# Optimization experiments

Hardware: AMD Instinct MI355X
Metric: run time of the kernel (lower is better)

## Reference

```python
import jax, jax.numpy as jnp
import numpy as np

EPS = 1e-5

def layer_norm(x, g, b):
    mu = jnp.mean(x, axis=-1, keepdims=True)
    var = jnp.var(x, axis=-1, keepdims=True)
    return (x - mu) * jax.lax.rsqrt(var + EPS) * g + b

def setup_inputs() -> dict:
    key = jax.random.key(0)
    ks = jax.random.split(key, 9)
    B, S, E = 16, 2048, 512
    H = 2 * E
    q = jax.random.normal(ks[0], (B, S, E), dtype=jnp.float32)
    k = jax.random.normal(ks[1], (B, S, E), dtype=jnp.float32)
    v = jax.random.normal(ks[2], (B, S, E), dtype=jnp.float32)
    # LayerNorm params (norm1 and norm3; norm2 is dead code in the original)
    ln1_g = jnp.ones((E,), jnp.float32); ln1_b = jnp.zeros((E,), jnp.float32)
    ln3_g = jnp.ones((E,), jnp.float32); ln3_b = jnp.zeros((E,), jnp.float32)
    # FFN params, torch Linear default init (uniform +- 1/sqrt(fan_in))
    lim1 = 1.0 / np.sqrt(E)
    w1 = jax.random.uniform(ks[3], (E, H), jnp.float32, -lim1, lim1)
    b1 = jax.random.uniform(ks[4], (H,), jnp.float32, -lim1, lim1)
    lim2 = 1.0 / np.sqrt(H)
    w2 = jax.random.uniform(ks[5], (H, E), jnp.float32, -lim2, lim2)
    b2 = jax.random.uniform(ks[6], (E,), jnp.float32, -lim2, lim2)
    return {"q": q, "k": k, "v": v, "ln1_g": ln1_g, "ln1_b": ln1_b,
            "w1": w1, "b1": b1, "w2": w2, "b2": b2,
            "ln3_g": ln3_g, "ln3_b": ln3_b}

def reference(q, k, v, ln1_g, ln1_b, w1, b1, w2, b2, ln3_g, ln3_b):
    # single-head full attention: scores [B,S,S]
    scale = 1.0 / jnp.sqrt(jnp.asarray(q.shape[-1], q.dtype))
    scores = jnp.einsum('bse,bte->bst', q, k) * scale
    attn = jax.nn.softmax(scores, axis=-1)
    attn_out = jnp.einsum('bst,bte->bse', attn, v)
    # residual + LayerNorm (dropout is identity at p=0 / eval)
    x = layer_norm(q + attn_out, ln1_g, ln1_b)
    # FFN: Linear -> exact GELU -> Linear
    h = jax.nn.gelu(jnp.einsum('bse,eh->bsh', x, w1) + b1, approximate=False)
    ff = jnp.einsum('bsh,he->bse', h, w2) + b2
    return layer_norm(x + ff, ln3_g, ln3_b)
```

## Files before the change

kernel.cpp:

```cpp
#include <hip/hip_runtime.h>
#include <cstdint>

#define B_ 16
#define S_ 2048
#define E_ 512
#define H_ 1024
#define SCALE 0.044194173824159216f
#define KVB 32
#define NTILES 64

typedef __attribute__((ext_vector_type(8))) short short8;
typedef __attribute__((ext_vector_type(4))) float floatx4;

static __device__ __forceinline__ unsigned short f2bf(float f) {
    unsigned u = __float_as_uint(f);
    u = u + 0x7FFFu + ((u >> 16) & 1u);
    return (unsigned short)(u >> 16);
}
static __device__ __forceinline__ float bf2f(unsigned short h) {
    return __uint_as_float(((unsigned)h) << 16);
}

__global__ void cvt_f32_bf16(const float* __restrict__ in, unsigned short* __restrict__ out, int n8) {
    int i = blockIdx.x * blockDim.x + threadIdx.x;
    if (i >= n8) return;
    const float4* p = (const float4*)in + (long)i * 2;
    float4 a = p[0], b = p[1];
    union { unsigned short u[8]; uint4 v; } r;
    r.u[0] = f2bf(a.x); r.u[1] = f2bf(a.y); r.u[2] = f2bf(a.z); r.u[3] = f2bf(a.w);
    r.u[4] = f2bf(b.x); r.u[5] = f2bf(b.y); r.u[6] = f2bf(b.z); r.u[7] = f2bf(b.w);
    ((uint4*)out)[i] = r.v;
}

__global__ void transpose_cvt(const float* __restrict__ in, unsigned short* __restrict__ out,
                              int R, int C, long inBS, long outBS) {
    __shared__ float t[64 * 68];
    const int z = blockIdx.z;
    in += (long)z * inBS; out += (long)z * outBS;
    const int c0 = blockIdx.x * 64, r0 = blockIdx.y * 64;
    const int tid = threadIdx.x;
    {
        int col4 = (tid & 15) * 4;
        #pragma unroll
        for (int i = 0; i < 4; i++) {
            int row = (tid >> 4) + i * 16;
            float4 v = *(const float4*)(in + (long)(r0 + row) * C + c0 + col4);
            *(float4*)(&t[row * 68 + col4]) = v;
        }
    }
    __syncthreads();
    {
        int oc = tid >> 2;
        int ob = (tid & 3) * 16;
        union { unsigned short u[16]; uint4 v[2]; } r;
        #pragma unroll
        for (int j = 0; j < 16; j++) r.u[j] = f2bf(t[(ob + j) * 68 + oc]);
        uint4* dst = (uint4*)(out + (long)(c0 + oc) * R + r0 + ob);
        dst[0] = r.v[0]; dst[1] = r.v[1];
    }
}

__launch_bounds__(256, 2)
__global__ void attn_kernel(const float* __restrict__ q,
                            const unsigned short* __restrict__ kb,
                            const unsigned short* __restrict__ vt,
                            const float* __restrict__ g1,
                            const float* __restrict__ bb1,
                            unsigned short* __restrict__ xb) {
    __shared__ unsigned short kLDS[2][KVB * E_];
    __shared__ unsigned short pLDS[64 * 40];
    __shared__ float aLDS[64];
    __shared__ float lLDS[64];
    __shared__ float sumLDS[64 * 4];
    __shared__ float sqLDS[64 * 4];
    const int tid = threadIdx.x;
    const int w = tid >> 6, lane = tid & 63, quad = lane >> 4, l16 = lane & 15;
    const int b = blockIdx.x >> 5, q0 = (blockIdx.x & 31) * 64;
    const floatx4 zf = {0.f, 0.f, 0.f, 0.f};

    const unsigned short* kb_b = kb + (long)b * S_ * E_;

    short8 aq[16];
    {
        const float* qp = q + (long)(b * S_ + q0 + 16 * w + l16) * E_ + quad * 8;
        #pragma unroll
        for (int kc = 0; kc < 16; kc++) {
            float4 x0 = *(const float4*)(qp + kc * 32);
            float4 x1 = *(const float4*)(qp + kc * 32 + 4);
            short8 t;
            t[0] = (short)f2bf(x0.x); t[1] = (short)f2bf(x0.y);
            t[2] = (short)f2bf(x0.z); t[3] = (short)f2bf(x0.w);
            t[4] = (short)f2bf(x1.x); t[5] = (short)f2bf(x1.y);
            t[6] = (short)f2bf(x1.z); t[7] = (short)f2bf(x1.w);
            aq[kc] = t;
        }
    }

    floatx4 oacc[4][8];
    #pragma unroll
    for (int qg = 0; qg < 4; qg++)
        #pragma unroll
        for (int nt = 0; nt < 8; nt++) oacc[qg][nt] = zf;
    float m_[4] = {-INFINITY, -INFINITY, -INFINITY, -INFINITY};
    float l_[4] = {0.f, 0.f, 0.f, 0.f};

    const unsigned short* vbase = vt + (long)(b * E_ + 128 * w + l16) * S_ + quad * 8;

    {
        #pragma unroll
        for (int j = 0; j < 8; j++) {
            int row = j * 4 + w;
            const unsigned short* g = kb_b + (long)row * E_ + ((lane * 8) ^ ((row & 7) << 3));
            __builtin_amdgcn_global_load_lds(
                (const __attribute__((address_space(1))) void*)g,
                (__attribute__((address_space(3))) void*)(&kLDS[0][row * E_]), 16, 0, 0);
        }
    }
    __syncthreads();

    for (int t = 0; t < NTILES; t++) {
        const int cur = t & 1;
        const int kt0 = t * KVB;

        if (t + 1 < NTILES) {
            const unsigned short* kb_t = kb_b + (long)(kt0 + KVB) * E_;
            #pragma unroll
            for (int j = 0; j < 8; j++) {
                int row = j * 4 + w;
                const unsigned short* g = kb_t + (long)row * E_ + ((lane * 8) ^ ((row & 7) << 3));
                __builtin_amdgcn_global_load_lds(
                    (const __attribute__((address_space(1))) void*)g,
                    (__attribute__((address_space(3))) void*)(&kLDS[cur ^ 1][row * E_]), 16, 0, 0);
            }
        }

        floatx4 sacc[2] = {zf, zf};
        const unsigned short* kl = &kLDS[cur][0];
        const int swz = (l16 & 7) << 3;
        #pragma unroll
        for (int kc = 0; kc < 16; kc++) {
            const int cx = (kc * 32 + quad * 8) ^ swz;
            short8 b0 = *(const short8*)(kl + l16 * E_ + cx);
            short8 b1 = *(const short8*)(kl + (16 + l16) * E_ + cx);
            sacc[0] = __builtin_amdgcn_mfma_f32_16x16x32_bf16(aq[kc], b0, sacc[0], 0, 0, 0);
            sacc[1] = __builtin_amdgcn_mfma_f32_16x16x32_bf16(aq[kc], b1, sacc[1], 0, 0, 0);
        }

        float rm[4], al[4], P2[2][4], rs[4];
        #pragma unroll
        for (int r = 0; r < 4; r++)
            rm[r] = fmaxf(sacc[0][r], sacc[1][r]) * SCALE;
        #pragma unroll
        for (int off = 1; off < 16; off <<= 1)
            #pragma unroll
            for (int r = 0; r < 4; r++) rm[r] = fmaxf(rm[r], __shfl_xor(rm[r], off));
        #pragma unroll
        for (int r = 0; r < 4; r++) {
            float mn = fmaxf(m_[r], rm[r]);
            al[r] = __expf(m_[r] - mn);
            m_[r] = mn;
            float p0 = __expf(sacc[0][r] * SCALE - mn);
            float p1 = __expf(sacc[1][r] * SCALE - mn);
            P2[0][r] = p0; P2[1][r] = p1;
            rs[r] = p0 + p1;
        }
        #pragma unroll
        for (int off = 1; off < 16; off <<= 1)
            #pragma unroll
            for (int r = 0; r < 4; r++) rs[r] += __shfl_xor(rs[r], off);
        #pragma unroll
        for (int r = 0; r < 4; r++) l_[r] = l_[r] * al[r] + rs[r];
        #pragma unroll
        for (int nt = 0; nt < 2; nt++)
            #pragma unroll
            for (int r = 0; r < 4; r++)
                pLDS[(16 * w + quad * 4 + r) * 40 + nt * 16 + l16] = f2bf(P2[nt][r]);
        if (l16 == 0) {
            #pragma unroll
            for (int r = 0; r < 4; r++) aLDS[16 * w + quad * 4 + r] = al[r];
        }
        __syncthreads();

        short8 pf[4];
        #pragma unroll
        for (int qg = 0; qg < 4; qg++)
            pf[qg] = *(const short8*)(&pLDS[(qg * 16 + l16) * 40 + quad * 8]);
        float av[4][4];
        #pragma unroll
        for (int qg = 0; qg < 4; qg++)
            #pragma unroll
            for (int r = 0; r < 4; r++) av[qg][r] = aLDS[qg * 16 + quad * 4 + r];
        #pragma unroll
        for (int qg = 0; qg < 4; qg++)
            #pragma unroll
            for (int nt = 0; nt < 8; nt++)
                #pragma unroll
                for (int r = 0; r < 4; r++) oacc[qg][nt][r] *= av[qg][r];
        const unsigned short* vtt = vbase + kt0;
        #pragma unroll
        for (int nt = 0; nt < 8; nt++) {
            short8 vf = *(const short8*)(vtt + (long)nt * 16 * S_);
            #pragma unroll
            for (int qg = 0; qg < 4; qg++)
                oacc[qg][nt] = __builtin_amdgcn_mfma_f32_16x16x32_bf16(pf[qg], vf, oacc[qg][nt], 0, 0, 0);
        }
        __syncthreads();
    }

    if (l16 == 0) {
        #pragma unroll
        for (int r = 0; r < 4; r++) lLDS[16 * w + quad * 4 + r] = l_[r];
    }
    __syncthreads();
    float lv[4][4];
    #pragma unroll
    for (int qg = 0; qg < 4; qg++)
        #pragma unroll
        for (int r = 0; r < 4; r++) lv[qg][r] = 1.f / lLDS[qg * 16 + quad * 4 + r];
    float ps[4][4], pq2[4][4];
    #pragma unroll
    for (int qg = 0; qg < 4; qg++)
        #pragma unroll
        for (int r = 0; r < 4; r++) { ps[qg][r] = 0.f; pq2[qg][r] = 0.f; }
    #pragma unroll
    for (int qg = 0; qg < 4; qg++)
        #pragma unroll
        for (int nt = 0; nt < 8; nt++)
            #pragma unroll
            for (int r = 0; r < 4; r++) {
                int qrow = q0 + qg * 16 + quad * 4 + r;
                int feat = 128 * w + nt * 16 + l16;
                float y = q[(long)(b * S_ + qrow) * E_ + feat] + oacc[qg][nt][r] * lv[qg][r];
                oacc[qg][nt][r] = y;
                ps[qg][r] += y; pq2[qg][r] += y * y;
            }
    #pragma unroll
    for (int off = 1; off < 16; off <<= 1)
        #pragma unroll
        for (int qg = 0; qg < 4; qg++)
            #pragma unroll
            for (int r = 0; r < 4; r++) {
                ps[qg][r] += __shfl_xor(ps[qg][r], off);
                pq2[qg][r] += __shfl_xor(pq2[qg][r], off);
            }
    if (l16 == 0) {
        #pragma unroll
        for (int qg = 0; qg < 4; qg++)
            #pragma unroll
            for (int r = 0; r < 4; r++) {
                int row = qg * 16 + quad * 4 + r;
                sumLDS[row * 4 + w] = ps[qg][r];
                sqLDS[row * 4 + w] = pq2[qg][r];
            }
    }
    __syncthreads();
    float mu[4][4], rstd[4][4];
    #pragma unroll
    for (int qg = 0; qg < 4; qg++)
        #pragma unroll
        for (int r = 0; r < 4; r++) {
            int row = qg * 16 + quad * 4 + r;
            float s = (sumLDS[row * 4 + 0] + sumLDS[row * 4 + 1]) + (sumLDS[row * 4 + 2] + sumLDS[row * 4 + 3]);
            float s2 = (sqLDS[row * 4 + 0] + sqLDS[row * 4 + 1]) + (sqLDS[row * 4 + 2] + sqLDS[row * 4 + 3]);
            float mean = s * (1.f / E_);
            float var = s2 * (1.f / E_) - mean * mean;
            mu[qg][r] = mean;
            rstd[qg][r] = rsqrtf(fmaxf(var, 0.f) + 1e-5f);
        }
    float gv[8], bv[8];
    #pragma unroll
    for (int nt = 0; nt < 8; nt++) {
        int feat = 128 * w + nt * 16 + l16;
        gv[nt] = g1[feat]; bv[nt] = bb1[feat];
    }
    #pragma unroll
    for (int qg = 0; qg < 4; qg++)
        #pragma unroll
        for (int nt = 0; nt < 8; nt++)
            #pragma unroll
            for (int r = 0; r < 4; r++) {
                int qrow = q0 + qg * 16 + quad * 4 + r;
                int feat = 128 * w + nt * 16 + l16;
                xb[(long)(b * S_ + qrow) * E_ + feat] =
                    f2bf((oacc[qg][nt][r] - mu[qg][r]) * rstd[qg][r] * gv[nt] + bv[nt]);
            }
}

__launch_bounds__(512, 2)
__global__ void ffn_ln3_kernel(const unsigned short* __restrict__ X,
                               const unsigned short* __restrict__ W1t,
                               const float* __restrict__ b1,
                               const unsigned short* __restrict__ W2t,
                               const float* __restrict__ b2,
                               const float* __restrict__ g3, const float* __restrict__ bb3,
                               float* __restrict__ Out) {
    __shared__ unsigned short ldsX[64 * 512];
    __shared__ unsigned short ldsH[2][64 * 256];
    __shared__ float sumLDS[64 * 8], sqLDS[64 * 8];
    const int tid = threadIdx.x, w = tid >> 6, lane = tid & 63, quad = lane >> 4, l16 = lane & 15;
    const long m0 = (long)blockIdx.x * 64;
    const floatx4 zf = {0.f, 0.f, 0.f, 0.f};
    floatx4 acc2[4][4];
    #pragma unroll
    for (int i = 0; i < 4; i++)
        #pragma unroll
        for (int j = 0; j < 4; j++) acc2[i][j] = zf;

    #pragma unroll
    for (int j = 0; j < 8; j++) {
        int row = w * 8 + j;
        const unsigned short* g = X + (m0 + row) * 512 + ((lane * 8) ^ ((row & 7) << 3));
        __builtin_amdgcn_global_load_lds(
            (const __attribute__((address_space(1))) void*)g,
            (__attribute__((address_space(3))) void*)(&ldsX[row * 512]), 16, 0, 0);
    }
    __syncthreads();

    const int swzx = (l16 & 7) << 3;
    for (int c = 0; c < 4; c++) {
        floatx4 acc1[4][2];
        #pragma unroll
        for (int mt = 0; mt < 4; mt++) { acc1[mt][0] = zf; acc1[mt][1] = zf; }
        const unsigned short* w1p = W1t + (long)(c * 256 + 32 * w + l16) * 512 + quad * 8;
        #pragma unroll
        for (int kc = 0; kc < 16; kc++) {
            short8 bf0 = *(const short8*)(w1p + kc * 32);
            short8 bf1 = *(const short8*)(w1p + 16 * 512 + kc * 32);
            const int cx = (kc * 32 + quad * 8) ^ swzx;
            #pragma unroll
            for (int mt = 0; mt < 4; mt++) {
                short8 af = *(const short8*)(&ldsX[(mt * 16 + l16) * 512 + cx]);
                acc1[mt][0] = __builtin_amdgcn_mfma_f32_16x16x32_bf16(af, bf0, acc1[mt][0], 0, 0, 0);
                acc1[mt][1] = __builtin_amdgcn_mfma_f32_16x16x32_bf16(af, bf1, acc1[mt][1], 0, 0, 0);
            }
        }
        unsigned short* hb = &ldsH[c & 1][0];
        #pragma unroll
        for (int nt = 0; nt < 2; nt++) {
            int hn = 32 * w + nt * 16 + l16;
            float b1v = b1[c * 256 + hn];
            int hc8 = hn >> 3, hoff = hn & 7;
            #pragma unroll
            for (int mt = 0; mt < 4; mt++)
                #pragma unroll
                for (int r = 0; r < 4; r++) {
                    int row = mt * 16 + quad * 4 + r;
                    float v = acc1[mt][nt][r] + b1v;
                    v = 0.5f * v * (1.f + erff(v * 0.70710678118f));
                    hb[row * 256 + ((hc8 ^ (row & 7)) << 3) + hoff] = f2bf(v);
                }
        }
        __syncthreads();

        const unsigned short* hrd = &ldsH[c & 1][0];
        const unsigned short* w2p = W2t + (long)(64 * w + l16) * 1024 + c * 256 + quad * 8;
        #pragma unroll
        for (int kc = 0; kc < 8; kc++) {
            short8 af[4], bf[4];
            const int hphys = ((kc * 4 + quad) ^ (l16 & 7)) << 3;
            #pragma unroll
            for (int mt = 0; mt < 4; mt++)
                af[mt] = *(const short8*)(&hrd[(mt * 16 + l16) * 256 + hphys]);
            #pragma unroll
            for (int nt = 0; nt < 4; nt++)
                bf[nt] = *(const short8*)(w2p + (long)nt * 16 * 1024 + kc * 32);
            #pragma unroll
            for (int mt = 0; mt < 4; mt++)
                #pragma unroll
                for (int nt = 0; nt < 4; nt++)
                    acc2[mt][nt] = __builtin_amdgcn_mfma_f32_16x16x32_bf16(af[mt], bf[nt], acc2[mt][nt], 0, 0, 0);
        }
    }

    float ps[4][4], pq2[4][4];
    #pragma unroll
    for (int mt = 0; mt < 4; mt++)
        #pragma unroll
        for (int r = 0; r < 4; r++) { ps[mt][r] = 0.f; pq2[mt][r] = 0.f; }
    #pragma unroll
    for (int nt = 0; nt < 4; nt++) {
        int n = 64 * w + nt * 16 + l16;
        float bv = b2[n];
        int nc8 = n >> 3, noff = n & 7;
        #pragma unroll
        for (int mt = 0; mt < 4; mt++)
            #pragma unroll
            for (int r = 0; r < 4; r++) {
                int row = mt * 16 + quad * 4 + r;
                float resid = bf2f(ldsX[row * 512 + ((nc8 ^ (row & 7)) << 3) + noff]);
                float v = acc2[mt][nt][r] + bv + resid;
                acc2[mt][nt][r] = v;
                ps[mt][r] += v; pq2[mt][r] += v * v;
            }
    }
    #pragma unroll
    for (int off = 1; off < 16; off <<= 1)
        #pragma unroll
        for (int mt = 0; mt < 4; mt++)
            #pragma unroll
            for (int r = 0; r < 4; r++) {
                ps[mt][r] += __shfl_xor(ps[mt][r], off);
                pq2[mt][r] += __shfl_xor(pq2[mt][r], off);
            }
    if (l16 == 0) {
        #pragma unroll
        for (int mt = 0; mt < 4; mt++)
            #pragma unroll
            for (int r = 0; r < 4; r++) {
                int row = mt * 16 + quad * 4 + r;
                sumLDS[row * 8 + w] = ps[mt][r];
                sqLDS[row * 8 + w] = pq2[mt][r];
            }
    }
    __syncthreads();
    float mu[4][4], rstd[4][4];
    #pragma unroll
    for (int mt = 0; mt < 4; mt++)
        #pragma unroll
        for (int r = 0; r < 4; r++) {
            int row = mt * 16 + quad * 4 + r;
            float s = 0.f, s2 = 0.f;
            #pragma unroll
            for (int ww = 0; ww < 8; ww++) { s += sumLDS[row * 8 + ww]; s2 += sqLDS[row * 8 + ww]; }
            float mean = s * (1.f / E_);
            float var = s2 * (1.f / E_) - mean * mean;
            mu[mt][r] = mean;
            rstd[mt][r] = rsqrtf(fmaxf(var, 0.f) + 1e-5f);
        }
    #pragma unroll
    for (int nt = 0; nt < 4; nt++) {
        int n = 64 * w + nt * 16 + l16;
        float gv = g3[n], bv3 = bb3[n];
        #pragma unroll
        for (int mt = 0; mt < 4; mt++) {
            long m = m0 + mt * 16 + quad * 4;
            #pragma unroll
            for (int r = 0; r < 4; r++)
                Out[(m + r) * E_ + n] =
                    (acc2[mt][nt][r] - mu[mt][r]) * rstd[mt][r] * gv + bv3;
        }
    }
}

extern "C" void kernel_launch(void* const* d_in, const int* in_sizes, int n_in,
                              void* d_out, int out_size, void* d_ws, size_t ws_size,
                              hipStream_t stream) {
    const float* q    = (const float*)d_in[0];
    const float* k    = (const float*)d_in[1];
    const float* v    = (const float*)d_in[2];
    const float* ln1g = (const float*)d_in[3];
    const float* ln1b = (const float*)d_in[4];
    const float* w1   = (const float*)d_in[5];
    const float* b1   = (const float*)d_in[6];
    const float* w2   = (const float*)d_in[7];
    const float* b2   = (const float*)d_in[8];
    const float* ln3g = (const float*)d_in[9];
    const float* ln3b = (const float*)d_in[10];

    char* ws = (char*)d_ws;
    unsigned short* kb  = (unsigned short*)(ws);
    unsigned short* vt  = (unsigned short*)(ws + 33554432);
    unsigned short* xb  = (unsigned short*)(ws + 67108864);
    unsigned short* w1t = (unsigned short*)(ws + 100663296);
    unsigned short* w2t = (unsigned short*)(ws + 101711872);
    float* ob = (float*)d_out;

    cvt_f32_bf16<<<8192, 256, 0, stream>>>(k, kb, 2097152);
    transpose_cvt<<<dim3(8, 32, 16), 256, 0, stream>>>(v, vt, 2048, 512, (long)2048 * 512, (long)512 * 2048);
    transpose_cvt<<<dim3(16, 8, 1), 256, 0, stream>>>(w1, w1t, 512, 1024, 0, 0);
    transpose_cvt<<<dim3(8, 16, 1), 256, 0, stream>>>(w2, w2t, 1024, 512, 0, 0);
    attn_kernel<<<512, 256, 0, stream>>>(q, kb, vt, ln1g, ln1b, xb);
    ffn_ln3_kernel<<<512, 512, 0, stream>>>(xb, w1t, b1, w2t, b2, ln3g, ln3b, ob);
}
```

Measured before the change: 807.1 us.

## Add lazy softmax rescaling and restructure FFN into smaller hidden chunks

The attention kernel now updates the running max only when a wave sees a new block max exceeding the old one by more than 8. When none do, it skips the exp for alpha and the accumulator rescale, using a per-wave flag in shared memory. The plain __syncthreads is replaced by an explicit waitcnt plus barrier. The FFN kernel splits the hidden dimension into 16 chunks of 64 instead of 4 of 256, with each wave computing one 16x32 GEMM1 tile. W2 fragments are prefetched before the barrier, LDS is shrunk and reused for the LayerNorm reductions, and occupancy is raised to 4 blocks per CU, at the cost of more barriers per block and smaller per-wave tiles.

```diff
diff --git a/kernel.cpp b/kernel.cpp
--- a/kernel.cpp
+++ b/kernel.cpp
@@ -70,6 +70,7 @@
     __shared__ unsigned short kLDS[2][KVB * E_];
     __shared__ unsigned short pLDS[64 * 40];
     __shared__ float aLDS[64];
+    __shared__ int fLDS[4];
     __shared__ float lLDS[64];
     __shared__ float sumLDS[64 * 4];
     __shared__ float sqLDS[64 * 4];
@@ -154,13 +155,23 @@
         for (int off = 1; off < 16; off <<= 1)
             #pragma unroll
             for (int r = 0; r < 4; r++) rm[r] = fmaxf(rm[r], __shfl_xor(rm[r], off));
+        bool resc = __any((rm[0] > m_[0] + 8.f) || (rm[1] > m_[1] + 8.f) ||
+                          (rm[2] > m_[2] + 8.f) || (rm[3] > m_[3] + 8.f));
+        if (resc) {
+            #pragma unroll
+            for (int r = 0; r < 4; r++) {
+                float mn = fmaxf(m_[r], rm[r]);
+                al[r] = __expf(m_[r] - mn);
+                m_[r] = mn;
+            }
+        } else {
+            #pragma unroll
+            for (int r = 0; r < 4; r++) al[r] = 1.f;
+        }
         #pragma unroll
         for (int r = 0; r < 4; r++) {
-            float mn = fmaxf(m_[r], rm[r]);
-            al[r] = __expf(m_[r] - mn);
-            m_[r] = mn;
-            float p0 = __expf(sacc[0][r] * SCALE - mn);
-            float p1 = __expf(sacc[1][r] * SCALE - mn);
+            float p0 = __expf(sacc[0][r] * SCALE - m_[r]);
+            float p1 = __expf(sacc[1][r] * SCALE - m_[r]);
             P2[0][r] = p0; P2[1][r] = p1;
             rs[r] = p0 + p1;
         }
@@ -179,23 +190,25 @@
             #pragma unroll
             for (int r = 0; r < 4; r++) aLDS[16 * w + quad * 4 + r] = al[r];
         }
-        __syncthreads();
+        if (lane == 0) fLDS[w] = resc ? 1 : 0;
+        asm volatile("s_waitcnt lgkmcnt(0)\n\ts_barrier" ::: "memory");
 
         short8 pf[4];
         #pragma unroll
         for (int qg = 0; qg < 4; qg++)
             pf[qg] = *(const short8*)(&pLDS[(qg * 16 + l16) * 40 + quad * 8]);
-        float av[4][4];
-        #pragma unroll
-        for (int qg = 0; qg < 4; qg++)
-            #pragma unroll
-            for (int r = 0; r < 4; r++) av[qg][r] = aLDS[qg * 16 + quad * 4 + r];
-        #pragma unroll
-        for (int qg = 0; qg < 4; qg++)
-            #pragma unroll
-            for (int nt = 0; nt < 8; nt++)
+        #pragma unroll
+        for (int qg = 0; qg < 4; qg++) {
+            if (fLDS[qg]) {
+                float av[4];
                 #pragma unroll
-                for (int r = 0; r < 4; r++) oacc[qg][nt][r] *= av[qg][r];
+                for (int r = 0; r < 4; r++) av[r] = aLDS[qg * 16 + quad * 4 + r];
+                #pragma unroll
+                for (int nt = 0; nt < 8; nt++)
+                    #pragma unroll
+                    for (int r = 0; r < 4; r++) oacc[qg][nt][r] *= av[r];
+            }
+        }
         const unsigned short* vtt = vbase + kt0;
         #pragma unroll
         for (int nt = 0; nt < 8; nt++) {
@@ -286,7 +299,7 @@
             }
 }
 
-__launch_bounds__(512, 2)
+__launch_bounds__(512, 4)
 __global__ void ffn_ln3_kernel(const unsigned short* __restrict__ X,
                                const unsigned short* __restrict__ W1t,
                                const float* __restrict__ b1,
@@ -295,8 +308,7 @@
                                const float* __restrict__ g3, const float* __restrict__ bb3,
                                float* __restrict__ Out) {
     __shared__ unsigned short ldsX[64 * 512];
-    __shared__ unsigned short ldsH[2][64 * 256];
-    __shared__ float sumLDS[64 * 8], sqLDS[64 * 8];
+    __shared__ unsigned short ldsH[64 * 64];
     const int tid = threadIdx.x, w = tid >> 6, lane = tid & 63, quad = lane >> 4, l16 = lane & 15;
     const long m0 = (long)blockIdx.x * 64;
     const floatx4 zf = {0.f, 0.f, 0.f, 0.f};
@@ -317,58 +329,52 @@
     __syncthreads();
 
     const int swzx = (l16 & 7) << 3;
-    for (int c = 0; c < 4; c++) {
-        floatx4 acc1[4][2];
-        #pragma unroll
-        for (int mt = 0; mt < 4; mt++) { acc1[mt][0] = zf; acc1[mt][1] = zf; }
-        const unsigned short* w1p = W1t + (long)(c * 256 + 32 * w + l16) * 512 + quad * 8;
+    const int mt1 = w & 3, nh = w >> 2;
+    for (int c = 0; c < 16; c++) {
+        floatx4 acc1[2] = {zf, zf};
+        const unsigned short* w1p = W1t + (long)(c * 64 + nh * 32 + l16) * 512 + quad * 8;
         #pragma unroll
         for (int kc = 0; kc < 16; kc++) {
             short8 bf0 = *(const short8*)(w1p + kc * 32);
             short8 bf1 = *(const short8*)(w1p + 16 * 512 + kc * 32);
-            const int cx = (kc * 32 + quad * 8) ^ swzx;
-            #pragma unroll
-            for (int mt = 0; mt < 4; mt++) {
-                short8 af = *(const short8*)(&ldsX[(mt * 16 + l16) * 512 + cx]);
-                acc1[mt][0] = __builtin_amdgcn_mfma_f32_16x16x32_bf16(af, bf0, acc1[mt][0], 0, 0, 0);
-                acc1[mt][1] = __builtin_amdgcn_mfma_f32_16x16x32_bf16(af, bf1, acc1[mt][1], 0, 0, 0);
-            }
-        }
-        unsigned short* hb = &ldsH[c & 1][0];
+            short8 af = *(const short8*)(&ldsX[(mt1 * 16 + l16) * 512 + ((kc * 32 + quad * 8) ^ swzx)]);
+            acc1[0] = __builtin_amdgcn_mfma_f32_16x16x32_bf16(af, bf0, acc1[0], 0, 0, 0);
+            acc1[1] = __builtin_amdgcn_mfma_f32_16x16x32_bf16(af, bf1, acc1[1], 0, 0, 0);
+        }
+        short8 w2f[2][4];
+        const unsigned short* w2p = W2t + (long)(64 * w + l16) * 1024 + c * 64 + quad * 8;
+        #pragma unroll
+        for (int kc = 0; kc < 2; kc++)
+            #pragma unroll
+            for (int nt = 0; nt < 4; nt++)
+                w2f[kc][nt] = *(const short8*)(w2p + (long)nt * 16 * 1024 + kc * 32);
+        __syncthreads();
         #pragma unroll
         for (int nt = 0; nt < 2; nt++) {
-            int hn = 32 * w + nt * 16 + l16;
-            float b1v = b1[c * 256 + hn];
-            int hc8 = hn >> 3, hoff = hn & 7;
+            int cc = nh * 32 + nt * 16 + l16;
+            float b1v = b1[c * 64 + cc];
+            int c8 = cc >> 3, coff = cc & 7;
+            #pragma unroll
+            for (int r = 0; r < 4; r++) {
+                int row = mt1 * 16 + quad * 4 + r;
+                float v = acc1[nt][r] + b1v;
+                v = 0.5f * v * (1.f + erff(v * 0.70710678118f));
+                ldsH[row * 64 + (((c8 ^ (row & 7)) << 3) + coff)] = f2bf(v);
+            }
+        }
+        __syncthreads();
+        #pragma unroll
+        for (int kc = 0; kc < 2; kc++) {
+            short8 af[4];
+            const int hphys = ((kc * 4 + quad) ^ (l16 & 7)) << 3;
             #pragma unroll
             for (int mt = 0; mt < 4; mt++)
-                #pragma unroll
-                for (int r = 0; r < 4; r++) {
-                    int row = mt * 16 + quad * 4 + r;
-                    float v = acc1[mt][nt][r] + b1v;
-                    v = 0.5f * v * (1.f + erff(v * 0.70710678118f));
-                    hb[row * 256 + ((hc8 ^ (row & 7)) << 3) + hoff] = f2bf(v);
-                }
-        }
-        __syncthreads();
-
-        const unsigned short* hrd = &ldsH[c & 1][0];
-        const unsigned short* w2p = W2t + (long)(64 * w + l16) * 1024 + c * 256 + quad * 8;
-        #pragma unroll
-        for (int kc = 0; kc < 8; kc++) {
-            short8 af[4], bf[4];
-            const int hphys = ((kc * 4 + quad) ^ (l16 & 7)) << 3;
-            #pragma unroll
-            for (int mt = 0; mt < 4; mt++)
-                af[mt] = *(const short8*)(&hrd[(mt * 16 + l16) * 256 + hphys]);
-            #pragma unroll
-            for (int nt = 0; nt < 4; nt++)
-                bf[nt] = *(const short8*)(w2p + (long)nt * 16 * 1024 + kc * 32);
+                af[mt] = *(const short8*)(&ldsH[(mt * 16 + l16) * 64 + hphys]);
             #pragma unroll
             for (int mt = 0; mt < 4; mt++)
                 #pragma unroll
                 for (int nt = 0; nt < 4; nt++)
-                    acc2[mt][nt] = __builtin_amdgcn_mfma_f32_16x16x32_bf16(af[mt], bf[nt], acc2[mt][nt], 0, 0, 0);
+                    acc2[mt][nt] = __builtin_amdgcn_mfma_f32_16x16x32_bf16(af[mt], w2f[kc][nt], acc2[mt][nt], 0, 0, 0);
         }
     }
 
@@ -387,7 +393,7 @@
             #pragma unroll
             for (int r = 0; r < 4; r++) {
                 int row = mt * 16 + quad * 4 + r;
-                float resid = bf2f(ldsX[row * 512 + ((nc8 ^ (row & 7)) << 3) + noff]);
+                float resid = bf2f(ldsX[row * 512 + (((nc8 ^ (row & 7)) << 3) + noff)]);
                 float v = acc2[mt][nt][r] + bv + resid;
                 acc2[mt][nt][r] = v;
                 ps[mt][r] += v; pq2[mt][r] += v * v;
@@ -402,14 +408,17 @@
                 ps[mt][r] += __shfl_xor(ps[mt][r], off);
                 pq2[mt][r] += __shfl_xor(pq2[mt][r], off);
             }
+    __syncthreads();
+    float* sumF = (float*)&ldsH[0];
+    float* sqF  = (float*)&ldsH[2048];
     if (l16 == 0) {
         #pragma unroll
         for (int mt = 0; mt < 4; mt++)
             #pragma unroll
             for (int r = 0; r < 4; r++) {
                 int row = mt * 16 + quad * 4 + r;
-                sumLDS[row * 8 + w] = ps[mt][r];
-                sqLDS[row * 8 + w] = pq2[mt][r];
+                sumF[row * 8 + w] = ps[mt][r];
+                sqF[row * 8 + w] = pq2[mt][r];
             }
     }
     __syncthreads();
@@ -421,7 +430,7 @@
             int row = mt * 16 + quad * 4 + r;
             float s = 0.f, s2 = 0.f;
             #pragma unroll
-            for (int ww = 0; ww < 8; ww++) { s += sumLDS[row * 8 + ww]; s2 += sqLDS[row * 8 + ww]; }
+            for (int ww = 0; ww < 8; ww++) { s += sumF[row * 8 + ww]; s2 += sqF[row * 8 + ww]; }
             float mean = s * (1.f / E_);
             float var = s2 * (1.f / E_) - mean * mean;
             mu[mt][r] = mean;
```

After: 1.088 ms. +34.8%, slower.
